# Kernel tuning notes

Measured on AMD Instinct MI355X. Metric: run time of the kernel, lower is better.

The kernel has to match this reference:

```python
import jax, jax.numpy as jnp
import numpy as np

NUM_GRAPHS = 512

def setup_inputs() -> dict:
    key = jax.random.key(0)
    ks = jax.random.split(key, 6)
    N, E, D = 100000, 1600000, 128
    x = jax.random.normal(ks[0], (N, D), dtype=jnp.float32)
    edge_index = jax.random.randint(ks[1], (2, E), 0, N, dtype=jnp.int64)
    batch = jnp.sort(jax.random.randint(ks[2], (N,), 0, NUM_GRAPHS, dtype=jnp.int64))
    scale = 1.0 / np.sqrt(D)
    Ws = jax.random.normal(ks[3], (4, D, D), dtype=jnp.float32) * scale
    bs = jnp.zeros((4, D), dtype=jnp.float32)
    Wl = jax.random.normal(ks[4], (D, 1), dtype=jnp.float32) * scale
    bl = jnp.zeros((1,), dtype=jnp.float32)
    return {"x": x, "edge_index": edge_index, "batch": batch,
            "Ws": Ws, "bs": bs, "Wl": Wl, "bl": bl}

def reference(x, edge_index, batch, Ws, bs, Wl, bl):
    N = x.shape[0]
    loops = jnp.arange(N, dtype=edge_index.dtype)
    # GCNConv: add self-loops, symmetric normalization D^{-1/2} A D^{-1/2}
    row = jnp.concatenate([edge_index[0], loops])  # source nodes
    col = jnp.concatenate([edge_index[1], loops])  # target nodes
    deg = jax.ops.segment_sum(jnp.ones_like(col, dtype=x.dtype), col, num_segments=N)
    dinv = jnp.where(deg > 0, jax.lax.rsqrt(jnp.maximum(deg, 1.0)), 0.0)
    norm = dinv[row] * dinv[col]  # [E+N]
    h = x
    for i in range(Ws.shape[0]):
        h = h @ Ws[i]                                   # [N, D]
        msg = h[row] * norm[:, None]                    # gather + scale, [E+N, D]
        h = jax.ops.segment_sum(msg, col, num_segments=N) + bs[i]
        h = jax.nn.relu(h)                              # dropout is identity in eval
    # global_mean_pool over graphs
    sums = jax.ops.segment_sum(h, batch, num_segments=NUM_GRAPHS)
    cnt = jax.ops.segment_sum(jnp.ones((N,), h.dtype), batch, num_segments=NUM_GRAPHS)
    pooled = sums / jnp.maximum(cnt, 1.0)[:, None]      # [G, D]
    return pooled @ Wl + bl                             # [G, 1]
```

## Files before the change

kernel.cpp:

```cpp
#include <hip/hip_runtime.h>


constexpr int D = 128;
constexpr int NGRAPH = 512;
constexpr int CHUNK = 2048;
constexpr int BSH = 9;
constexpr int OP = 136;

typedef __attribute__((ext_vector_type(8))) short bf16x8;
typedef __attribute__((ext_vector_type(4))) float f32x4;
typedef int i32x4u __attribute__((ext_vector_type(4), aligned(4)));

__device__ __forceinline__ float bf2f(unsigned short b) {
    return __uint_as_float(((unsigned int)b) << 16);
}
__device__ __forceinline__ unsigned short f2bf(float f) {
    unsigned int u = __float_as_uint(f);
    u += 0x7FFFu + ((u >> 16) & 1u);
    return (unsigned short)(u >> 16);
}

__global__ __launch_bounds__(256) void setup_all(
        const float4* __restrict__ x4, ushort4* __restrict__ hb, int n4, int CB,
        const float* __restrict__ W, unsigned short* __restrict__ Wt,
        const int* __restrict__ ec, int E, int* __restrict__ bucketCnt) {
    __shared__ int h[256];
    const int t = threadIdx.x;
    const int b = blockIdx.x;
    if (b < CB) {
        int i = b * 256 + t;
        if (i < n4) {
            float4 v = x4[i];
            ushort4 o;
            o.x = f2bf(v.x); o.y = f2bf(v.y); o.z = f2bf(v.z); o.w = f2bf(v.w);
            hb[i] = o;
        }
    } else if (b < CB + 256) {
        int idx = (b - CB) * 256 + t;
        int i = idx >> 14;
        int rem = idx & 16383;
        int k = rem >> 7, c = rem & 127;
        Wt[(i << 14) + c * 128 + k] = f2bf(W[idx]);
    } else {
        h[t] = 0;
        __syncthreads();
        const int e0 = (b - CB - 256) * CHUNK;
        const int cnt = min(CHUNK, E - e0);
        for (int i = t; i < cnt; i += 256) atomicAdd(&h[ec[e0 + i] >> BSH], 1);
        __syncthreads();
        if (h[t]) atomicAdd(&bucketCnt[t], h[t]);
    }
}

__global__ __launch_bounds__(256) void bucket_scan(const int* __restrict__ bucketCnt,
                                                   int* __restrict__ bucketBase,
                                                   int* __restrict__ globCursor) {
    __shared__ int s[256];
    const int t = threadIdx.x;
    int v = bucketCnt[t];
    s[t] = v; __syncthreads();
    for (int off = 1; off < 256; off <<= 1) {
        int x = (t >= off) ? s[t - off] : 0;
        __syncthreads();
        s[t] += x;
        __syncthreads();
    }
    int excl = s[t] - v;
    bucketBase[t] = excl;
    globCursor[t] = excl;
}

__global__ __launch_bounds__(256) void scatter_pairs(const int* __restrict__ er,
                                                     const int* __restrict__ ec, int E,
                                                     int* __restrict__ globCursor,
                                                     int* __restrict__ pairs) {
    __shared__ int h[256], lbase[256], cur[256], segd[256], s[256];
    __shared__ int stage[CHUNK];
    __shared__ unsigned char sb[CHUNK];
    const int t = threadIdx.x;
    const int e0 = blockIdx.x * CHUNK;
    const int cnt = min(CHUNK, E - e0);

    h[t] = 0;
    __syncthreads();
    for (int i = t; i < cnt; i += 256) atomicAdd(&h[ec[e0 + i] >> BSH], 1);
    __syncthreads();
    int v = h[t];
    s[t] = v; __syncthreads();
    for (int off = 1; off < 256; off <<= 1) {
        int x = (t >= off) ? s[t - off] : 0;
        __syncthreads();
        s[t] += x;
        __syncthreads();
    }
    lbase[t] = s[t] - v;
    cur[t] = s[t] - v;
    segd[t] = atomicAdd(&globCursor[t], v) - lbase[t];
    __syncthreads();
    for (int i = t; i < cnt; i += 256) {
        int c = ec[e0 + i];
        int b = c >> BSH;
        int p = atomicAdd(&cur[b], 1);
        stage[p] = (er[e0 + i] << BSH) | (c & 511);
        sb[p] = (unsigned char)b;
    }
    __syncthreads();
    for (int i = t; i < cnt; i += 256) {
        int b = sb[i];
        pairs[segd[b] + i] = stage[i];
    }
}

__global__ __launch_bounds__(256) void fill_csr(const int* __restrict__ pairs,
                                                const int* __restrict__ bucketBase,
                                                const int* __restrict__ bucketCnt,
                                                int N, int E, int NBUCK,
                                                int* __restrict__ rowptr,
                                                float* __restrict__ dinv,
                                                int* __restrict__ srcs) {
    __shared__ int hist[512], lofs[512], s[256];
    const int t = threadIdx.x;
    const int b = blockIdx.x;
    const int c0 = b << BSH;
    const int base = bucketBase[b];
    const int cnt = bucketCnt[b];
    const int* pp = pairs + base;

    hist[t] = 0; hist[t + 256] = 0;
    __syncthreads();
    for (int i = t; i < cnt; i += 256) atomicAdd(&hist[pp[i] & 511], 1);
    __syncthreads();
    int a0 = hist[2 * t], a1 = hist[2 * t + 1];
    s[t] = a0 + a1; __syncthreads();
    for (int off = 1; off < 256; off <<= 1) {
        int x = (t >= off) ? s[t - off] : 0;
        __syncthreads();
        s[t] += x;
        __syncthreads();
    }
    int excl = s[t] - (a0 + a1);
    lofs[2 * t] = excl;
    lofs[2 * t + 1] = excl + a0;
    __syncthreads();
    const int nn = min(512, N - c0);
    for (int i = t; i < nn; i += 256) {
        rowptr[c0 + i] = base + lofs[i];
        dinv[c0 + i] = rsqrtf((float)hist[i] + 1.0f);
    }
    if (b == NBUCK - 1 && t == 0) rowptr[N] = E;
    __syncthreads();
    for (int i = t; i < cnt; i += 256) {
        int pr = pp[i];
        int p = atomicAdd(&lofs[pr & 511], 1);
        srcs[base + p] = pr >> BSH;
    }
}

__global__ __launch_bounds__(256) void scale_x(uint4* __restrict__ Hb0,
                                               const float* __restrict__ dinv,
                                               int nq) {
    int i = blockIdx.x * 256 + threadIdx.x;
    if (i >= nq) return;
    float dv = dinv[i >> 4];
    uint4 v = Hb0[i];
    unsigned int* p = (unsigned int*)&v;
#pragma unroll
    for (int k = 0; k < 4; ++k) {
        unsigned int d = p[k];
        unsigned short lo = f2bf(bf2f((unsigned short)(d & 0xFFFFu)) * dv);
        unsigned short hi = f2bf(bf2f((unsigned short)(d >> 16)) * dv);
        p[k] = ((unsigned int)hi << 16) | lo;
    }
    Hb0[i] = v;
}

__global__ __launch_bounds__(256, 4) void layer_fused(
        const int* __restrict__ rowptr, const int* __restrict__ srcs,
        const float* __restrict__ dinv, const unsigned short* __restrict__ H,
        const unsigned short* __restrict__ Wt, const float* __restrict__ bias,
        unsigned short* __restrict__ Hn, float* __restrict__ dots,
        const float* __restrict__ Wl, int N, int writeDots) {
    __shared__ __align__(16) unsigned short U[16 * OP];
    const int tid = threadIdx.x;
    const int wave = tid >> 6;
    const int lane = tid & 63;
    const int row16 = lane & 15;
    const int quad = lane >> 4;
    const int grp = wave * 4 + quad;
    const int r0 = blockIdx.x * 16;
    const bf16x8* H8 = (const bf16x8*)H;
    const int gl = row16;

    {
        const int rt = grp;
        const int row = r0 + rt;
        float acc[8] = {0.f, 0.f, 0.f, 0.f, 0.f, 0.f, 0.f, 0.f};
        float sn = 0.f;
        if (row < N) {
            sn = dinv[row];
            int j = rowptr[row];
            const int end = rowptr[row + 1];
            bf16x8 hv = H8[(size_t)row * 16 + gl];
#pragma unroll
            for (int k = 0; k < 8; ++k) acc[k] = bf2f((unsigned short)hv[k]);
            const int ne = end - j;
            const int nb = (ne + 7) >> 3;
            if (nb > 0) {
                i32x4u sA0, sA1, sB0, sB1;
                {
                    const i32x4u* sp = (const i32x4u*)(srcs + j);
                    sA0 = sp[0]; sA1 = sp[1];
                }
                if (nb > 1) {
                    const i32x4u* sp = (const i32x4u*)(srcs + j + 8);
                    sB0 = sp[0]; sB1 = sp[1];
                }
                bf16x8 hc[8], hn[8];
#pragma unroll
                for (int t = 0; t < 8; ++t) {
                    int idx = (t < 4) ? sA0[t] : sA1[t - 4];
                    int rr = (t < ne) ? idx : row;
                    hc[t] = H8[(size_t)rr * 16 + gl];
                }
#pragma unroll 1
                for (int b = 0; b < nb; ++b) {
                    if (b + 1 < nb) {
                        const int remn = ne - (b + 1) * 8;
                        int rn[8];
#pragma unroll
                        for (int t = 0; t < 8; ++t) {
                            int idx = (t < 4) ? sB0[t] : sB1[t - 4];
                            rn[t] = (t < remn) ? idx : row;
                        }
                        if (b + 2 < nb) {
                            const i32x4u* sp = (const i32x4u*)(srcs + j + (b + 2) * 8);
                            sB0 = sp[0]; sB1 = sp[1];
                        }
#pragma unroll
                        for (int t = 0; t < 8; ++t)
                            hn[t] = H8[(size_t)rn[t] * 16 + gl];
                    }
                    const int rem = ne - b * 8;
#pragma unroll
                    for (int t = 0; t < 8; ++t) {
                        const float w = (t < rem) ? 1.f : 0.f;
#pragma unroll
                        for (int k = 0; k < 8; ++k)
                            acc[k] = fmaf(w, bf2f((unsigned short)hc[t][k]), acc[k]);
                    }
#pragma unroll
                    for (int t = 0; t < 8; ++t) hc[t] = hn[t];
                }
            }
        }
        bf16x8 o;
#pragma unroll
        for (int k = 0; k < 8; ++k) o[k] = (short)f2bf(sn * acc[k]);
        *(bf16x8*)(U + rt * 128 + ((gl ^ rt) << 3)) = o;
    }
    __syncthreads();

    bf16x8 a0[4];
#pragma unroll
    for (int kc = 0; kc < 4; ++kc) {
        const int ph = (kc * 4 + quad) ^ row16;
        a0[kc] = *(const bf16x8*)(U + row16 * 128 + ph * 8);
    }
    __syncthreads();

    float dv[4];
    if (!writeDots) {
#pragma unroll
        for (int i = 0; i < 4; ++i) {
            int ra = r0 + quad * 4 + i;
            dv[i] = (ra < N) ? dinv[ra] : 0.f;
        }
    }

    float rd[4] = {0.f, 0.f, 0.f, 0.f};
#pragma unroll
    for (int c = 0; c < 2; ++c) {
        const int ct = wave * 2 + c;
        const int col = ct * 16 + row16;
        const bf16x8* wc = (const bf16x8*)(Wt + (size_t)col * 128);
        f32x4 acc0 = {0.f, 0.f, 0.f, 0.f};
#pragma unroll
        for (int kc = 0; kc < 4; ++kc) {
            const bf16x8 wf = wc[kc * 4 + quad];
            acc0 = __builtin_amdgcn_mfma_f32_16x16x32_bf16(a0[kc], wf, acc0, 0, 0, 0);
        }
        const float bv = bias[col];
        if (writeDots) {
            const float wl = Wl[col];
#pragma unroll
            for (int i = 0; i < 4; ++i) rd[i] += fmaxf(acc0[i] + bv, 0.f) * wl;
        } else {
#pragma unroll
            for (int i = 0; i < 4; ++i)
                U[(quad * 4 + i) * OP + col] = f2bf(dv[i] * fmaxf(acc0[i] + bv, 0.f));
        }
    }

    if (writeDots) {
#pragma unroll
        for (int m = 1; m < 16; m <<= 1)
#pragma unroll
            for (int i = 0; i < 4; ++i) rd[i] += __shfl_xor(rd[i], m, 64);
        float* R = (float*)U;
        if (row16 == 0) {
#pragma unroll
            for (int i = 0; i < 4; ++i) R[wave * 16 + quad * 4 + i] = rd[i];
        }
        __syncthreads();
        if (tid < 16) dots[r0 + tid] = R[tid] + R[16 + tid] + R[32 + tid] + R[48 + tid];
    } else {
        __syncthreads();
        {
            int row = tid >> 4, c8 = tid & 15;
            bf16x8 v = *(const bf16x8*)(U + row * OP + c8 * 8);
            *(bf16x8*)(Hn + (size_t)(r0 + row) * 128 + c8 * 8) = v;
        }
    }
}

__global__ __launch_bounds__(256) void pool_graphs(const float* __restrict__ dots,
                                                   const int* __restrict__ batch, int N,
                                                   const float* __restrict__ bl,
                                                   float* __restrict__ out) {
    __shared__ int bounds[2];
    __shared__ float red[4];
    const int g = blockIdx.x;
    const int t = threadIdx.x;
    if (t < 2) {
        int key = g + t;
        int lo = 0, hi = N;
        while (lo < hi) {
            int mid = (lo + hi) >> 1;
            if (batch[mid] < key) lo = mid + 1; else hi = mid;
        }
        bounds[t] = lo;
    }
    __syncthreads();
    const int lo = bounds[0], hi = bounds[1];
    float s = 0.f;
    for (int i = lo + t; i < hi; i += 256) s += dots[i];
#pragma unroll
    for (int off = 32; off > 0; off >>= 1) s += __shfl_down(s, off, 64);
    if ((t & 63) == 0) red[t >> 6] = s;
    __syncthreads();
    if (t == 0) {
        float tot = red[0] + red[1] + red[2] + red[3];
        int cnt = hi - lo;
        out[g] = tot / (float)(cnt > 0 ? cnt : 1) + bl[0];
    }
}

extern "C" void kernel_launch(void* const* d_in, const int* in_sizes, int n_in,
                              void* d_out, int out_size, void* d_ws, size_t ws_size,
                              hipStream_t stream) {
    const float* x     = (const float*)d_in[0];
    const int*   eidx  = (const int*)d_in[1];
    const int*   batch = (const int*)d_in[2];
    const float* Ws    = (const float*)d_in[3];
    const float* bs    = (const float*)d_in[4];
    const float* Wl    = (const float*)d_in[5];
    const float* bl    = (const float*)d_in[6];
    (void)n_in; (void)out_size;

    const int N = in_sizes[0] / D;
    const int E = in_sizes[1] / 2;
    const int* er = eidx;
    const int* ec = eidx + E;
    const int NBUCK = (N + 511) >> BSH;
    const int NCHUNK = (E + CHUNK - 1) / CHUNK;

    const int Npad = (N + 127) & ~127;
    const size_t hBytes = (size_t)Npad * D * sizeof(unsigned short);
    auto al = [](size_t v) { return (v + 255) & ~(size_t)255; };
    char* base = (char*)d_ws;
    size_t off = 0;

    unsigned short* Hb0 = (unsigned short*)base; off = al(hBytes);
    int* bucketCnt  = (int*)(base + off);
    int* globCursor = bucketCnt + 256;
    off = al(off + 512 * sizeof(int));
    int*   bucketBase = (int*)(base + off);  off = al(off + 256 * sizeof(int));
    float* dinv   = (float*)(base + off);    off = al(off + (size_t)Npad * sizeof(float));
    float* dots   = (float*)(base + off);    off = al(off + (size_t)Npad * sizeof(float));
    int*   rowptr = (int*)(base + off);      off = al(off + (size_t)(Npad + 64) * sizeof(int));
    int*   srcs   = (int*)(base + off);      off = al(off + ((size_t)E + 64) * sizeof(int));
    unsigned short* Wt = (unsigned short*)(base + off);   off = al(off + 4 * 128 * 128 * sizeof(unsigned short));

    const bool twoBuf = ws_size >= off + hBytes;
    unsigned short* Hb1 = twoBuf ? (unsigned short*)(base + off)
                                 : (unsigned short*)d_in[0];
    int* pairs = (int*)Hb1;
    unsigned short* hb[2] = { Hb0, Hb1 };

    hipMemsetAsync(bucketCnt, 0, 256 * sizeof(int), stream);
    const int n4 = N * D / 4;
    const int CB = (n4 + 255) / 256;
    setup_all<<<CB + 256 + NCHUNK, 256, 0, stream>>>((const float4*)x, (ushort4*)Hb0,
                                                     n4, CB, Ws, Wt, ec, E, bucketCnt);

    bucket_scan<<<1, 256, 0, stream>>>(bucketCnt, bucketBase, globCursor);
    scatter_pairs<<<NCHUNK, 256, 0, stream>>>(er, ec, E, globCursor, pairs);
    fill_csr<<<NBUCK, 256, 0, stream>>>(pairs, bucketBase, bucketCnt, N, E, NBUCK,
                                        rowptr, dinv, srcs);
    const int nq = N * 16;
    scale_x<<<(nq + 255) / 256, 256, 0, stream>>>((uint4*)Hb0, dinv, nq);

    for (int i = 0; i < 4; ++i) {
        const unsigned short* Hc = hb[i & 1];
        unsigned short* Hn = hb[(i + 1) & 1];
        layer_fused<<<Npad / 16, 256, 0, stream>>>(rowptr, srcs, dinv, Hc,
                                                   Wt + (size_t)i * D * D,
                                                   bs + (size_t)i * D, Hn, dots, Wl,
                                                   N, (i == 3) ? 1 : 0);
    }

    pool_graphs<<<NGRAPH, 256, 0, stream>>>(dots, batch, N, bl, (float*)d_out);
}
```

Before: 450.0 us.

## Split neighbor aggregation across two thread halves; fold dinv scaling into setup

Result: slower. 583.5 us (+29.7%).

```diff
diff --git a/kernel.cpp b/kernel.cpp
--- a/kernel.cpp
+++ b/kernel.cpp
@@ -20,19 +20,30 @@
     return (unsigned short)(u >> 16);
 }
 
+__global__ __launch_bounds__(256) void count_deg(const int* __restrict__ ec, int E,
+                                                 int* __restrict__ deg) {
+    int i = blockIdx.x * 256 + threadIdx.x;
+    const int stride = gridDim.x * 256;
+    for (; i < E; i += stride) atomicAdd(&deg[ec[i]], 1);
+}
+
 __global__ __launch_bounds__(256) void setup_all(
         const float4* __restrict__ x4, ushort4* __restrict__ hb, int n4, int CB,
         const float* __restrict__ W, unsigned short* __restrict__ Wt,
-        const int* __restrict__ ec, int E, int* __restrict__ bucketCnt) {
+        const int* __restrict__ ec, int E, int* __restrict__ bucketCnt,
+        const int* __restrict__ deg) {
     __shared__ int h[256];
     const int t = threadIdx.x;
     const int b = blockIdx.x;
     if (b < CB) {
         int i = b * 256 + t;
         if (i < n4) {
+            const int node = i >> 5;
+            const float dv = rsqrtf((float)deg[node] + 1.0f);
             float4 v = x4[i];
             ushort4 o;
-            o.x = f2bf(v.x); o.y = f2bf(v.y); o.z = f2bf(v.z); o.w = f2bf(v.w);
+            o.x = f2bf(v.x * dv); o.y = f2bf(v.y * dv);
+            o.z = f2bf(v.z * dv); o.w = f2bf(v.w * dv);
             hb[i] = o;
         }
     } else if (b < CB + 256) {
@@ -156,56 +167,45 @@
     }
 }
 
-__global__ __launch_bounds__(256) void scale_x(uint4* __restrict__ Hb0,
-                                               const float* __restrict__ dinv,
-                                               int nq) {
-    int i = blockIdx.x * 256 + threadIdx.x;
-    if (i >= nq) return;
-    float dv = dinv[i >> 4];
-    uint4 v = Hb0[i];
-    unsigned int* p = (unsigned int*)&v;
-#pragma unroll
-    for (int k = 0; k < 4; ++k) {
-        unsigned int d = p[k];
-        unsigned short lo = f2bf(bf2f((unsigned short)(d & 0xFFFFu)) * dv);
-        unsigned short hi = f2bf(bf2f((unsigned short)(d >> 16)) * dv);
-        p[k] = ((unsigned int)hi << 16) | lo;
-    }
-    Hb0[i] = v;
-}
-
-__global__ __launch_bounds__(256, 4) void layer_fused(
+__global__ __launch_bounds__(512, 4) void layer_fused(
         const int* __restrict__ rowptr, const int* __restrict__ srcs,
         const float* __restrict__ dinv, const unsigned short* __restrict__ H,
         const unsigned short* __restrict__ Wt, const float* __restrict__ bias,
         unsigned short* __restrict__ Hn, float* __restrict__ dots,
         const float* __restrict__ Wl, int N, int writeDots) {
     __shared__ __align__(16) unsigned short U[16 * OP];
+    __shared__ float F[16][128];
     const int tid = threadIdx.x;
     const int wave = tid >> 6;
     const int lane = tid & 63;
     const int row16 = lane & 15;
     const int quad = lane >> 4;
-    const int grp = wave * 4 + quad;
+    const int grp = tid >> 4;
+    const int rt = grp & 15;
+    const int hf = grp >> 4;
+    const int gl = tid & 15;
     const int r0 = blockIdx.x * 16;
     const bf16x8* H8 = (const bf16x8*)H;
-    const int gl = row16;
 
     {
-        const int rt = grp;
         const int row = r0 + rt;
         float acc[8] = {0.f, 0.f, 0.f, 0.f, 0.f, 0.f, 0.f, 0.f};
-        float sn = 0.f;
         if (row < N) {
-            sn = dinv[row];
-            int j = rowptr[row];
-            const int end = rowptr[row + 1];
-            bf16x8 hv = H8[(size_t)row * 16 + gl];
-#pragma unroll
-            for (int k = 0; k < 8; ++k) acc[k] = bf2f((unsigned short)hv[k]);
-            const int ne = end - j;
-            const int nb = (ne + 7) >> 3;
-            if (nb > 0) {
+            const int j0 = rowptr[row];
+            const int neF = rowptr[row + 1] - j0;
+            const int nbF = (neF + 7) >> 3;
+            const int nb0 = (nbF + 1) >> 1;
+            const int bs = hf ? nb0 : 0;
+            const int be = hf ? nbF : nb0;
+            const int j = j0 + bs * 8;
+            const int ne = min(neF, be * 8) - bs * 8;
+            if (hf == 0) {
+                bf16x8 hv = H8[(size_t)row * 16 + gl];
+#pragma unroll
+                for (int k = 0; k < 8; ++k) acc[k] = bf2f((unsigned short)hv[k]);
+            }
+            const int nb = be - bs;
+            if (ne > 0 && nb > 0) {
                 i32x4u sA0, sA1, sB0, sB1;
                 {
                     const i32x4u* sp = (const i32x4u*)(srcs + j);
@@ -253,10 +253,19 @@
                 }
             }
         }
-        bf16x8 o;
-#pragma unroll
-        for (int k = 0; k < 8; ++k) o[k] = (short)f2bf(sn * acc[k]);
-        *(bf16x8*)(U + rt * 128 + ((gl ^ rt) << 3)) = o;
+        if (hf == 1) {
+#pragma unroll
+            for (int k = 0; k < 8; ++k) F[rt][gl * 8 + k] = acc[k];
+        }
+        __syncthreads();
+        if (hf == 0) {
+            const float sn = (row < N) ? dinv[row] : 0.f;
+            bf16x8 o;
+#pragma unroll
+            for (int k = 0; k < 8; ++k)
+                o[k] = (short)f2bf(sn * (acc[k] + F[rt][gl * 8 + k]));
+            *(bf16x8*)(U + rt * 128 + ((gl ^ rt) << 3)) = o;
+        }
     }
     __syncthreads();
 
@@ -268,19 +277,18 @@
     }
     __syncthreads();
 
-    float dv[4];
+    float dv4[4];
     if (!writeDots) {
 #pragma unroll
         for (int i = 0; i < 4; ++i) {
             int ra = r0 + quad * 4 + i;
-            dv[i] = (ra < N) ? dinv[ra] : 0.f;
+            dv4[i] = (ra < N) ? dinv[ra] : 0.f;
         }
     }
 
     float rd[4] = {0.f, 0.f, 0.f, 0.f};
-#pragma unroll
-    for (int c = 0; c < 2; ++c) {
-        const int ct = wave * 2 + c;
+    {
+        const int ct = wave;
         const int col = ct * 16 + row16;
         const bf16x8* wc = (const bf16x8*)(Wt + (size_t)col * 128);
         f32x4 acc0 = {0.f, 0.f, 0.f, 0.f};
@@ -297,7 +305,7 @@
         } else {
 #pragma unroll
             for (int i = 0; i < 4; ++i)
-                U[(quad * 4 + i) * OP + col] = f2bf(dv[i] * fmaxf(acc0[i] + bv, 0.f));
+                U[(quad * 4 + i) * OP + col] = f2bf(dv4[i] * fmaxf(acc0[i] + bv, 0.f));
         }
     }
 
@@ -306,16 +314,22 @@
         for (int m = 1; m < 16; m <<= 1)
 #pragma unroll
             for (int i = 0; i < 4; ++i) rd[i] += __shfl_xor(rd[i], m, 64);
-        float* R = (float*)U;
+        float* R = &F[0][0];
+        __syncthreads();
         if (row16 == 0) {
 #pragma unroll
             for (int i = 0; i < 4; ++i) R[wave * 16 + quad * 4 + i] = rd[i];
         }
         __syncthreads();
-        if (tid < 16) dots[r0 + tid] = R[tid] + R[16 + tid] + R[32 + tid] + R[48 + tid];
+        if (tid < 16) {
+            float s = 0.f;
+#pragma unroll
+            for (int w = 0; w < 8; ++w) s += R[w * 16 + tid];
+            dots[r0 + tid] = s;
+        }
     } else {
         __syncthreads();
-        {
+        if (tid < 256) {
             int row = tid >> 4, c8 = tid & 15;
             bf16x8 v = *(const bf16x8*)(U + row * OP + c8 * 8);
             *(bf16x8*)(Hn + (size_t)(r0 + row) * 128 + c8 * 8) = v;
@@ -387,6 +401,7 @@
     int*   bucketBase = (int*)(base + off);  off = al(off + 256 * sizeof(int));
     float* dinv   = (float*)(base + off);    off = al(off + (size_t)Npad * sizeof(float));
     float* dots   = (float*)(base + off);    off = al(off + (size_t)Npad * sizeof(float));
+    int*   deg    = (int*)(base + off);      off = al(off + (size_t)Npad * sizeof(int));
     int*   rowptr = (int*)(base + off);      off = al(off + (size_t)(Npad + 64) * sizeof(int));
     int*   srcs   = (int*)(base + off);      off = al(off + ((size_t)E + 64) * sizeof(int));
     unsigned short* Wt = (unsigned short*)(base + off);   off = al(off + 4 * 128 * 128 * sizeof(unsigned short));
@@ -398,22 +413,23 @@
     unsigned short* hb[2] = { Hb0, Hb1 };
 
     hipMemsetAsync(bucketCnt, 0, 256 * sizeof(int), stream);
+    hipMemsetAsync(deg, 0, (size_t)Npad * sizeof(int), stream);
+    count_deg<<<min((E + 255) / 256, 2048), 256, 0, stream>>>(ec, E, deg);
     const int n4 = N * D / 4;
     const int CB = (n4 + 255) / 256;
     setup_all<<<CB + 256 + NCHUNK, 256, 0, stream>>>((const float4*)x, (ushort4*)Hb0,
-                                                     n4, CB, Ws, Wt, ec, E, bucketCnt);
+                                                     n4, CB, Ws, Wt, ec, E, bucketCnt,
+                                                     deg);
 
     bucket_scan<<<1, 256, 0, stream>>>(bucketCnt, bucketBase, globCursor);
     scatter_pairs<<<NCHUNK, 256, 0, stream>>>(er, ec, E, globCursor, pairs);
     fill_csr<<<NBUCK, 256, 0, stream>>>(pairs, bucketBase, bucketCnt, N, E, NBUCK,
                                         rowptr, dinv, srcs);
-    const int nq = N * 16;
-    scale_x<<<(nq + 255) / 256, 256, 0, stream>>>((uint4*)Hb0, dinv, nq);
 
     for (int i = 0; i < 4; ++i) {
         const unsigned short* Hc = hb[i & 1];
         unsigned short* Hn = hb[(i + 1) & 1];
-        layer_fused<<<Npad / 16, 256, 0, stream>>>(rowptr, srcs, dinv, Hc,
+        layer_fused<<<Npad / 16, 512, 0, stream>>>(rowptr, srcs, dinv, Hc,
                                                    Wt + (size_t)i * D * D,
                                                    bs + (size_t)i * D, Hn, dots, Wl,
                                                    N, (i == 3) ? 1 : 0);
```
